# Performance work log

Hardware: AMD Instinct MI355X
Metric: run time of the kernel (lower is better)

Reference implementation:

```python
import jax, jax.numpy as jnp
import numpy as np

DIM = 1024
N_HEADS = 16
HEAD_DIM = DIM // N_HEADS
SCALE = HEAD_DIM ** 0.5


def setup_inputs() -> dict:
    key = jax.random.key(0)
    k_x, k_wqkv, k_bqkv, k_wp, k_bp = jax.random.split(key, 5)
    B, S = 4, 2048
    x = jax.random.normal(k_x, (B, S, DIM), dtype=jnp.float32)
    # Linear params stored input-major: y = x @ W + b
    std_qkv = 1.0 / np.sqrt(DIM)
    W_qkv = jax.random.uniform(k_wqkv, (DIM, 3 * DIM), jnp.float32, -std_qkv, std_qkv)
    b_qkv = jax.random.uniform(k_bqkv, (3 * DIM,), jnp.float32, -std_qkv, std_qkv)
    W_proj = jax.random.uniform(k_wp, (DIM, DIM), jnp.float32, -std_qkv, std_qkv)
    b_proj = jax.random.uniform(k_bp, (DIM,), jnp.float32, -std_qkv, std_qkv)
    return {"x": x, "W_qkv": W_qkv, "b_qkv": b_qkv, "W_proj": W_proj, "b_proj": b_proj}


def reference(x, W_qkv, b_qkv, W_proj, b_proj):
    B, S, D = x.shape
    qkv = x @ W_qkv + b_qkv                       # [B,S,3D]
    Q, K, V = jnp.split(qkv, 3, axis=-1)          # each [B,S,D]
    def heads(t):                                 # [B,S,D] -> [B,H,S,hd]
        return t.reshape(B, S, N_HEADS, HEAD_DIM).transpose(0, 2, 1, 3)
    Q, K, V = heads(Q), heads(K), heads(V)
    scores = jnp.einsum('bhqd,bhkd->bhqk', Q, K) / SCALE   # [B,H,S,S]
    attn = jax.nn.softmax(scores, axis=-1)
    out = jnp.einsum('bhqk,bhkd->bhqd', attn, V)           # [B,H,S,hd]
    out = out.transpose(0, 2, 1, 3).reshape(B, S, D)
    return out @ W_proj + b_proj
```

## Files before the change

### kernel.cpp

```cpp
#include <hip/hip_runtime.h>
#include <hip/hip_bf16.h>

typedef __attribute__((ext_vector_type(8))) __bf16 bf16x8;
typedef __attribute__((ext_vector_type(4))) float f32x4;
typedef __attribute__((ext_vector_type(16))) float f32x16;
typedef __attribute__((ext_vector_type(4))) unsigned int u32x4;

#define DIM 1024
#define NHEADS 16
#define HDIM 64
#define BATCH 4
#define SEQ 2048
#define ROWS (BATCH * SEQ)
#define SCL 0.18033688011112042f

__device__ inline unsigned short f2bf(float f) {
    __hip_bfloat16 h = __float2bfloat16(f);
    return *reinterpret_cast<unsigned short*>(&h);
}

__device__ inline unsigned int packbf2(float a, float b) {
    unsigned short ua = __builtin_bit_cast(unsigned short, (__bf16)a);
    unsigned short ub = __builtin_bit_cast(unsigned short, (__bf16)b);
    return (unsigned int)ua | ((unsigned int)ub << 16);
}

typedef const __attribute__((address_space(1))) unsigned int* gas_ptr;
typedef __attribute__((address_space(3))) unsigned int* las_ptr;
__device__ inline void gload16(const void* g, void* l) {
    __builtin_amdgcn_global_load_lds((gas_ptr)g, (las_ptr)l, 16, 0, 0);
}

__global__ __launch_bounds__(256) void prologue(const float* __restrict__ x,
                                                unsigned short* __restrict__ x_bf,
                                                const float* __restrict__ W_qkv,
                                                unsigned short* __restrict__ WqkvT,
                                                const float* __restrict__ W_proj,
                                                unsigned short* __restrict__ WprojT) {
    __shared__ float tile[32][33];
    const int blk = blockIdx.x;
    if (blk < 8192) {
        int i = blk * 256 + threadIdx.x;
        float4 v = ((const float4*)x)[i];
        ushort4 o;
        o.x = f2bf(v.x); o.y = f2bf(v.y); o.z = f2bf(v.z); o.w = f2bf(v.w);
        ((ushort4*)x_bf)[i] = o;
        return;
    }
    const float* in; unsigned short* outp; int C, srows, bx, byy; float scl;
    if (blk < 11264) {
        int t = blk - 8192;
        in = W_qkv; outp = WqkvT; C = 3 * DIM; srows = DIM; scl = SCL;
        bx = t % 96; byy = t / 96;
    } else {
        int t = blk - 11264;
        in = W_proj; outp = WprojT; C = DIM; srows = 0; scl = 1.f;
        bx = t & 31; byy = t >> 5;
    }
    const int R = DIM;
    int c0 = bx * 32, r0 = byy * 32;
    int tx = threadIdx.x & 31, ty = threadIdx.x >> 5;
#pragma unroll
    for (int i = 0; i < 32; i += 8) {
        int r = r0 + ty + i, c = c0 + tx;
        tile[ty + i][tx] = in[(size_t)r * C + c];
    }
    __syncthreads();
#pragma unroll
    for (int i = 0; i < 32; i += 8) {
        int orow = c0 + ty + i, oc = r0 + tx;
        float v = tile[tx][ty + i];
        if (orow < srows) v *= scl;
        outp[(size_t)orow * R + oc] = f2bf(v);
    }
}

__global__ __launch_bounds__(512, 2) void qkv_gemm_pack(const unsigned short* __restrict__ A,
                                                        const unsigned short* __restrict__ Bt,
                                                        const float* __restrict__ bias,
                                                        unsigned short* __restrict__ Cq,
                                                        unsigned short* __restrict__ Kp,
                                                        unsigned short* __restrict__ Vp) {
    __shared__ __align__(16) char SMEM[131072];
    const int tid = threadIdx.x;
    const int lane = tid & 63, wave = tid >> 6;
    const int wr = wave >> 2, wc = wave & 3;
    const int fr = lane & 15, lh = lane >> 4;
    const int gflat = blockIdx.y * gridDim.x + blockIdx.x;
    const int bidx = (gflat & 7) * 48 + (gflat >> 3);
    const int bx = bidx % 12, byy = bidx / 12;
    const int rowA = byy * 256, colB = bx * 256;

    const int sA = wave * 8 + (lane >> 3);
    const int arow0 = sA;
    const int crow0 = (sA & 31) + (sA >> 5) * 64;
    const int glb = ((lane & 7) ^ (lane >> 3)) * 16;
    const int ga0 = ((lh) ^ (fr & 7)) * 16;
    const int ga1 = ((4 + lh) ^ (fr & 7)) * 16;
    const int aoff = (wr * 64 + fr) * 128;
    const int boff = (wc * 32 + fr) * 128;

    f32x4 acc[8][4] = {};

    auto stA = [&](int tb, int h, int tt) {
        char* d = SMEM + tb * 65536 + h * 16384 + wave * 1024;
        const char* g0 = (const char*)A +
            (((size_t)(rowA + arow0 + h * 64)) * 1024 + (size_t)tt * 64) * 2 + glb;
        gload16(g0, d);
        gload16(g0 + (size_t)128 * 2048, d + 8192);
    };
    auto stB = [&](int tb, int h, int tt) {
        char* d = SMEM + tb * 65536 + 32768 + h * 16384 + wave * 1024;
        const char* g0 = (const char*)Bt +
            (((size_t)(colB + crow0 + h * 32)) * 1024 + (size_t)tt * 64) * 2 + glb;
        gload16(g0, d);
        gload16(g0 + (size_t)128 * 2048, d + 8192);
    };

    stA(0, 0, 0); stB(0, 0, 0); stA(0, 1, 0); stB(0, 1, 0);
    stA(1, 0, 1); stB(1, 0, 1);
    asm volatile("s_waitcnt vmcnt(4)" ::: "memory");
    __builtin_amdgcn_s_barrier();

    bf16x8 afq[4][2];
    for (int u = 0; u < 16; ++u) {
        const int cur = u & 1;
        const char* Al = SMEM + cur * 65536;
        const char* Bl = SMEM + cur * 65536 + 32768;
        {
            bf16x8 bfp[2][2];
#pragma unroll
            for (int i = 0; i < 4; i++) {
                afq[i][0] = *(const bf16x8*)(Al + aoff + i * 2048 + ga0);
                afq[i][1] = *(const bf16x8*)(Al + aoff + i * 2048 + ga1);
            }
#pragma unroll
            for (int j = 0; j < 2; j++) {
                bfp[j][0] = *(const bf16x8*)(Bl + boff + j * 2048 + ga0);
                bfp[j][1] = *(const bf16x8*)(Bl + boff + j * 2048 + ga1);
            }
            if (u + 1 < 16) stA(cur ^ 1, 1, u + 1);
            __builtin_amdgcn_s_barrier();
            __builtin_amdgcn_s_setprio(1);
#pragma unroll
            for (int i = 0; i < 4; i++)
#pragma unroll
                for (int j = 0; j < 2; j++) {
                    acc[i][j] = __builtin_amdgcn_mfma_f32_16x16x32_bf16(afq[i][0], bfp[j][0], acc[i][j], 0, 0, 0);
                    acc[i][j] = __builtin_amdgcn_mfma_f32_16x16x32_bf16(afq[i][1], bfp[j][1], acc[i][j], 0, 0, 0);
                }
            __builtin_amdgcn_s_setprio(0);
            __builtin_amdgcn_s_barrier();
        }
        {
            bf16x8 bfp[2][2];
#pragma unroll
            for (int j = 0; j < 2; j++) {
                bfp[j][0] = *(const bf16x8*)(Bl + 16384 + boff + j * 2048 + ga0);
                bfp[j][1] = *(const bf16x8*)(Bl + 16384 + boff + j * 2048 + ga1);
            }
            if (u + 1 < 16) stB(cur ^ 1, 1, u + 1);
            __builtin_amdgcn_s_barrier();
            __builtin_amdgcn_s_setprio(1);
#pragma unroll
            for (int i = 0; i < 4; i++)
#pragma unroll
                for (int j = 0; j < 2; j++) {
                    acc[i][2 + j] = __builtin_amdgcn_mfma_f32_16x16x32_bf16(afq[i][0], bfp[j][0], acc[i][2 + j], 0, 0, 0);
                    acc[i][2 + j] = __builtin_amdgcn_mfma_f32_16x16x32_bf16(afq[i][1], bfp[j][1], acc[i][2 + j], 0, 0, 0);
                }
            __builtin_amdgcn_s_setprio(0);
            __builtin_amdgcn_s_barrier();
        }
        {
            bf16x8 bfp[2][2];
#pragma unroll
            for (int i = 0; i < 4; i++) {
                afq[i][0] = *(const bf16x8*)(Al + 16384 + aoff + i * 2048 + ga0);
                afq[i][1] = *(const bf16x8*)(Al + 16384 + aoff + i * 2048 + ga1);
            }
#pragma unroll
            for (int j = 0; j < 2; j++) {
                bfp[j][0] = *(const bf16x8*)(Bl + boff + j * 2048 + ga0);
                bfp[j][1] = *(const bf16x8*)(Bl + boff + j * 2048 + ga1);
            }
            if (u + 2 < 16) stA(cur, 0, u + 2);
            __builtin_amdgcn_s_barrier();
            __builtin_amdgcn_s_setprio(1);
#pragma unroll
            for (int i = 0; i < 4; i++)
#pragma unroll
                for (int j = 0; j < 2; j++) {
                    acc[4 + i][j] = __builtin_amdgcn_mfma_f32_16x16x32_bf16(afq[i][0], bfp[j][0], acc[4 + i][j], 0, 0, 0);
                    acc[4 + i][j] = __builtin_amdgcn_mfma_f32_16x16x32_bf16(afq[i][1], bfp[j][1], acc[4 + i][j], 0, 0, 0);
                }
            __builtin_amdgcn_s_setprio(0);
            __builtin_amdgcn_s_barrier();
        }
        {
            bf16x8 bfp[2][2];
#pragma unroll
            for (int j = 0; j < 2; j++) {
                bfp[j][0] = *(const bf16x8*)(Bl + 16384 + boff + j * 2048 + ga0);
                bfp[j][1] = *(const bf16x8*)(Bl + 16384 + boff + j * 2048 + ga1);
            }
            if (u + 2 < 16) stB(cur, 0, u + 2);
            __builtin_amdgcn_s_barrier();
            __builtin_amdgcn_s_setprio(1);
#pragma unroll
            for (int i = 0; i < 4; i++)
#pragma unroll
                for (int j = 0; j < 2; j++) {
                    acc[4 + i][2 + j] = __builtin_amdgcn_mfma_f32_16x16x32_bf16(afq[i][0], bfp[j][0], acc[4 + i][2 + j], 0, 0, 0);
                    acc[4 + i][2 + j] = __builtin_amdgcn_mfma_f32_16x16x32_bf16(afq[i][1], bfp[j][1], acc[4 + i][2 + j], 0, 0, 0);
                }
            __builtin_amdgcn_s_setprio(0);
            if (u < 14) asm volatile("s_waitcnt vmcnt(4)" ::: "memory");
            else        asm volatile("s_waitcnt vmcnt(0)" ::: "memory");
            __builtin_amdgcn_s_barrier();
        }
    }

    const int cm = (lane >> 4) * 4, cn = lane & 15;
    const int gn0 = colB + wc * 64;
    if (gn0 < 1024) {
        for (int ni = 0; ni < 4; ni++) {
            int gn = gn0 + ni * 16 + cn;
            float bv = bias[gn] * SCL;
            for (int mi = 0; mi < 8; mi++) {
#pragma unroll
                for (int r = 0; r < 4; r++) {
                    int gm = rowA + wr * 128 + mi * 16 + cm + r;
                    Cq[(size_t)gm * 1024 + gn] = f2bf(acc[mi][ni][r] + bv);
                }
            }
        }
    } else {
        const int mm = lane & 31, hh = lane >> 5;
        unsigned short* Lw = (unsigned short*)SMEM + wave * (64 * 72);
        for (int kg = 0; kg < 2; kg++) {
            for (int ni = 0; ni < 4; ni++) {
                float bv = bias[gn0 + ni * 16 + cn];
                for (int mi = 0; mi < 4; mi++) {
#pragma unroll
                    for (int r = 0; r < 4; r++)
                        Lw[(mi * 16 + cm + r) * 72 + ni * 16 + cn] =
                            f2bf(acc[kg * 4 + mi][ni][r] + bv);
                }
            }
            __builtin_amdgcn_s_waitcnt(0);
            const int keybase = rowA + wr * 128 + kg * 64;
            const int b = keybase >> 11, s0g = keybase & 2047;
            if (gn0 < 2048) {
                const int h = (gn0 - 1024) >> 6;
                const size_t by = (size_t)(b * 16 + h);
                const int kub = s0g >> 5;
#pragma unroll
                for (int f = 0; f < 8; f++) {
                    int ktl = f >> 2, ks = f & 3;
                    uint4 d = *(const uint4*)&Lw[(ktl * 32 + mm) * 72 + ks * 16 + hh * 8];
                    *(uint4*)(Kp + ((by * 64 + kub + ktl) * 4 + ks) * 512 + lane * 8) = d;
                }
            } else {
                const int h = (gn0 - 2048) >> 6;
                const size_t by = (size_t)(b * 16 + h);
                const int vub = s0g >> 4;
#pragma unroll
                for (int f = 0; f < 8; f++) {
                    int ksl = f >> 1, dt = f & 1;
                    unsigned short tmp[8];
#pragma unroll
                    for (int j = 0; j < 8; j++)
                        tmp[j] = Lw[(ksl * 16 + (j & 3) + 8 * (j >> 2) + 4 * hh) * 72 + dt * 32 + mm];
                    *(uint4*)(Vp + ((by * 128 + vub + ksl) * 2 + dt) * 512 + lane * 8) =
                        *(uint4*)tmp;
                }
            }
            __builtin_amdgcn_s_waitcnt(0);
        }
    }
}

__global__ __launch_bounds__(256) void gemm_bt_bias(const unsigned short* __restrict__ A,
                                                    const unsigned short* __restrict__ Bt,
                                                    const float* __restrict__ bias,
                                                    float* __restrict__ Cf,
                                                    int M, int N, int K) {
    __shared__ unsigned short SMEM[16384];
    unsigned short* As0 = SMEM;
    unsigned short* Bs0 = SMEM + 8192;
    const int tid = threadIdx.x;
    const int lane = tid & 63, wave = tid >> 6;
    const int wm = (wave >> 1) * 64, wn = (wave & 1) * 64;
    const int nwg = gridDim.x * gridDim.y;
    const int gflat = blockIdx.y * gridDim.x + blockIdx.x;
    const int bidx = (gflat & 7) * (nwg >> 3) + (gflat >> 3);
    const int bx = bidx % gridDim.x, byy = bidx / gridDim.x;
    const int rowA = byy * 128, rowB = bx * 128;
    const int fr = lane & 15, fo = (lane >> 4) * 8;

    f32x4 acc[4][4] = {};

    for (int k0 = 0; k0 < K; k0 += 64) {
#pragma unroll
        for (int kc = 0; kc < 2; kc++) {
#pragma unroll
            for (int c = 0; c < 2; c++) {
                int o = c * 4096 + tid * 16;
                int r = o >> 6, cb = o & 63;
                int ldsb = c * 4096 + wave * 1024;
                gload16((const char*)A + ((size_t)(rowA + r) * K + k0 + kc * 32) * 2 + cb,
                        (char*)As0 + kc * 8192 + ldsb);
                gload16((const char*)Bt + ((size_t)(rowB + r) * K + k0 + kc * 32) * 2 + cb,
                        (char*)Bs0 + kc * 8192 + ldsb);
            }
        }
        __syncthreads();
#pragma unroll
        for (int kc = 0; kc < 2; kc++) {
            bf16x8 af[4], bfr[4];
#pragma unroll
            for (int i = 0; i < 4; i++) {
                af[i]  = *(const bf16x8*)(As0 + kc * 4096 + (wm + i * 16 + fr) * 32 + fo);
                bfr[i] = *(const bf16x8*)(Bs0 + kc * 4096 + (wn + i * 16 + fr) * 32 + fo);
            }
#pragma unroll
            for (int mi = 0; mi < 4; mi++)
#pragma unroll
                for (int ni = 0; ni < 4; ni++)
                    acc[mi][ni] = __builtin_amdgcn_mfma_f32_16x16x32_bf16(af[mi], bfr[ni],
                                                                          acc[mi][ni], 0, 0, 0);
        }
        __syncthreads();
    }

    const int cn = lane & 15, cm = (lane >> 4) * 4;
    for (int ni = 0; ni < 4; ni++) {
        int gn = rowB + wn + ni * 16 + cn;
        float bv = bias[gn];
        for (int mi = 0; mi < 4; mi++) {
#pragma unroll
            for (int r = 0; r < 4; r++) {
                int gm = rowA + wm + mi * 16 + cm + r;
                Cf[(size_t)gm * N + gn] = acc[mi][ni][r] + bv;
            }
        }
    }
}

__device__ inline void softmax_pv(const f32x16& cfrag, const bf16x8 vf[2][2],
                                  f32x16& o0, f32x16& o1, float& psum) {
    unsigned int pk[8];
    float es[8];
#pragma unroll
    for (int p = 0; p < 8; p++) {
        float e0 = __builtin_amdgcn_exp2f(cfrag[2 * p]);
        float e1 = __builtin_amdgcn_exp2f(cfrag[2 * p + 1]);
        es[p] = e0 + e1;
        pk[p] = packbf2(e0, e1);
    }
    psum += ((es[0] + es[1]) + (es[2] + es[3])) + ((es[4] + es[5]) + (es[6] + es[7]));
    u32x4 lo = {pk[0], pk[1], pk[2], pk[3]};
    u32x4 hi = {pk[4], pk[5], pk[6], pk[7]};
    bf16x8 pa0 = __builtin_bit_cast(bf16x8, lo);
    bf16x8 pa1 = __builtin_bit_cast(bf16x8, hi);
    o0 = __builtin_amdgcn_mfma_f32_32x32x16_bf16(pa0, vf[0][0], o0, 0, 0, 0);
    o1 = __builtin_amdgcn_mfma_f32_32x32x16_bf16(pa0, vf[0][1], o1, 0, 0, 0);
    o0 = __builtin_amdgcn_mfma_f32_32x32x16_bf16(pa1, vf[1][0], o0, 0, 0, 0);
    o1 = __builtin_amdgcn_mfma_f32_32x32x16_bf16(pa1, vf[1][1], o1, 0, 0, 0);
}

__device__ inline void attn_step(const bf16x8 kf[4], const bf16x8 vf[2][2],
                                 const bf16x8 qf[2][4], f32x16 oacc[2][2], float psum[2]) {
    f32x16 cf0 = {}, cf1 = {};
#pragma unroll
    for (int ks = 0; ks < 4; ks++)
        cf0 = __builtin_amdgcn_mfma_f32_32x32x16_bf16(kf[ks], qf[0][ks], cf0, 0, 0, 0);
#pragma unroll
    for (int ks = 0; ks < 4; ks++)
        cf1 = __builtin_amdgcn_mfma_f32_32x32x16_bf16(kf[ks], qf[1][ks], cf1, 0, 0, 0);
    softmax_pv(cf0, vf, oacc[0][0], oacc[0][1], psum[0]);
    softmax_pv(cf1, vf, oacc[1][0], oacc[1][1], psum[1]);
}

__global__ __launch_bounds__(256, 2) void attn_kernel(const unsigned short* __restrict__ Qb,
                                                      const unsigned short* __restrict__ Kp,
                                                      const unsigned short* __restrict__ Vp,
                                                      unsigned short* __restrict__ attnb) {
    __shared__ float Po[2][8 * 256];
    __shared__ float Pl[2][128];
    const int tid = threadIdx.x;
    const int lane = tid & 63, wave = tid >> 6;
    const int qpair = wave >> 1, ksplit = wave & 1;
    const int m31 = lane & 31, h = lane >> 5;
    const int gflat = blockIdx.y * gridDim.x + blockIdx.x;
    const int xcd = gflat & 7, slot = gflat >> 3;
    const int by = xcd * 8 + (slot >> 4);
    const int qb = slot & 15;
    const int b = by >> 4;
    const int bS = b * SEQ, hcol = (by & 15) * HDIM;
    const int q0 = qb * 128 + qpair * 64;

    bf16x8 qf[2][4];
#pragma unroll
    for (int qt = 0; qt < 2; qt++)
#pragma unroll
        for (int ks = 0; ks < 4; ks++)
            qf[qt][ks] = *(const bf16x8*)(Qb + (size_t)(bS + q0 + qt * 32 + m31) * 1024 +
                                          hcol + ks * 16 + h * 8);

    f32x16 oacc[2][2] = {};
    float psum[2] = {0.f, 0.f};

    const unsigned short* kbase = Kp + (size_t)by * 64 * 2048 + lane * 8;
    const unsigned short* vbase = Vp + (size_t)by * 128 * 1024 + lane * 8;

    const int ku0 = ksplit * 32;
    bf16x8 kfa[4], kfb[4];
    {
        const unsigned short* kp = kbase + (size_t)ku0 * 2048;
#pragma unroll
        for (int ks = 0; ks < 4; ks++) kfa[ks] = *(const bf16x8*)(kp + ks * 512);
    }
    for (int ki = 0; ki < 32; ki += 2) {
        {
            int ku = ku0 + ki;
            bf16x8 vf[2][2];
#pragma unroll
            for (int ks = 0; ks < 2; ks++) {
                const unsigned short* vp = vbase + ((size_t)ku * 2 + ks) * 1024;
                vf[ks][0] = *(const bf16x8*)(vp);
                vf[ks][1] = *(const bf16x8*)(vp + 512);
            }
            const unsigned short* kpn = kbase + (size_t)(ku + 1) * 2048;
#pragma unroll
            for (int ks = 0; ks < 4; ks++) kfb[ks] = *(const bf16x8*)(kpn + ks * 512);
            attn_step(kfa, vf, qf, oacc, psum);
        }
        {
            int ku = ku0 + ki + 1;
            bf16x8 vf[2][2];
#pragma unroll
            for (int ks = 0; ks < 2; ks++) {
                const unsigned short* vp = vbase + ((size_t)ku * 2 + ks) * 1024;
                vf[ks][0] = *(const bf16x8*)(vp);
                vf[ks][1] = *(const bf16x8*)(vp + 512);
            }
            int kup = ku0 + ((ki + 2 < 32) ? (ki + 2) : 31);
            const unsigned short* kpn = kbase + (size_t)kup * 2048;
#pragma unroll
            for (int ks = 0; ks < 4; ks++) kfa[ks] = *(const bf16x8*)(kpn + ks * 512);
            attn_step(kfb, vf, qf, oacc, psum);
        }
    }

#pragma unroll
    for (int qt = 0; qt < 2; qt++) {
        if (ksplit == 1) {
#pragma unroll
            for (int dt = 0; dt < 2; dt++)
#pragma unroll
                for (int c = 0; c < 4; c++) {
                    f32x4 v = {oacc[qt][dt][c * 4 + 0], oacc[qt][dt][c * 4 + 1],
                               oacc[qt][dt][c * 4 + 2], oacc[qt][dt][c * 4 + 3]};
                    *(f32x4*)&Po[qpair][(dt * 4 + c) * 256 + lane * 4] = v;
                }
            if (qt == 0)
                *(float2*)&Pl[qpair][lane * 2] = make_float2(psum[0], psum[1]);
        }
        __syncthreads();
        if (ksplit == 0) {
#pragma unroll
            for (int dt = 0; dt < 2; dt++)
#pragma unroll
                for (int c = 0; c < 4; c++) {
                    f32x4 v = *(const f32x4*)&Po[qpair][(dt * 4 + c) * 256 + lane * 4];
#pragma unroll
                    for (int j = 0; j < 4; j++) oacc[qt][dt][c * 4 + j] += v[j];
                }
            if (qt == 0) {
                float2 pl = *(const float2*)&Pl[qpair][lane * 2];
                psum[0] += pl.x; psum[1] += pl.y;
            }
        }
        if (qt == 0) __syncthreads();
    }

    if (ksplit == 0) {
#pragma unroll
        for (int qt = 0; qt < 2; qt++) {
            float lt = psum[qt] + __shfl_xor(psum[qt], 32, 64);
            float rl = 1.f / lt;
#pragma unroll
            for (int r = 0; r < 16; r++) {
                int row = (r & 3) + 8 * (r >> 2) + 4 * h;
                float rlr = __shfl(rl, row, 64);
                size_t orow = (size_t)(bS + q0 + qt * 32 + row) * 1024 + hcol;
                attnb[orow + m31]      = f2bf(oacc[qt][0][r] * rlr);
                attnb[orow + 32 + m31] = f2bf(oacc[qt][1][r] * rlr);
            }
        }
    }
}

extern "C" void kernel_launch(void* const* d_in, const int* in_sizes, int n_in,
                              void* d_out, int out_size, void* d_ws, size_t ws_size,
                              hipStream_t stream) {
    const float* x      = (const float*)d_in[0];
    const float* W_qkv  = (const float*)d_in[1];
    const float* b_qkv  = (const float*)d_in[2];
    const float* W_proj = (const float*)d_in[3];
    const float* b_proj = (const float*)d_in[4];
    float* out = (float*)d_out;

    char* ws = (char*)d_ws;
    unsigned short* x_bf   = (unsigned short*)(ws);
    unsigned short* WqkvT  = (unsigned short*)(ws + 16777216);
    unsigned short* Qb     = (unsigned short*)(ws + 23068672);
    unsigned short* Kp     = (unsigned short*)(ws + 39845888);
    unsigned short* Vp     = (unsigned short*)(ws + 56623104);
    unsigned short* WprojT = (unsigned short*)(ws + 73400320);
    unsigned short* attnb  = (unsigned short*)(ws);

    prologue<<<12288, 256, 0, stream>>>(x, x_bf, W_qkv, WqkvT, W_proj, WprojT);

    qkv_gemm_pack<<<dim3(12, 32), 512, 0, stream>>>(x_bf, WqkvT, b_qkv, Qb, Kp, Vp);

    attn_kernel<<<dim3(SEQ / 128, BATCH * NHEADS), 256, 0, stream>>>(Qb, Kp, Vp, attnb);

    gemm_bt_bias<<<dim3(DIM / 128, ROWS / 128), 256, 0, stream>>>(
        attnb, WprojT, b_proj, out, ROWS, DIM, DIM);
}
```

Measured before the change: 257.3 us.

## Unify QKV and output-projection GEMMs into one pipelined 256x128-tile kernel

The QKV GEMM tile shrinks from 256x256 to 256x128, with 8 waves laid out 4x2 and 96KB of LDS, which doubles the QKV grid to 24x32 workgroups. The same software-pipelined kernel now also runs the output projection (8x32 grid, fp32 output plus bias), replacing the simpler non-pipelined 128x128 gemm_bt_bias. The goals are better CU occupancy and load balance for the QKV GEMM, and a faster output projection through double-buffered async loads. The trade-off is lower per-tile data reuse.

```diff
diff --git a/kernel.cpp b/kernel.cpp
--- a/kernel.cpp
+++ b/kernel.cpp
@@ -75,62 +75,62 @@
     }
 }
 
-__global__ __launch_bounds__(512, 2) void qkv_gemm_pack(const unsigned short* __restrict__ A,
-                                                        const unsigned short* __restrict__ Bt,
-                                                        const float* __restrict__ bias,
-                                                        unsigned short* __restrict__ Cq,
-                                                        unsigned short* __restrict__ Kp,
-                                                        unsigned short* __restrict__ Vp) {
-    __shared__ __align__(16) char SMEM[131072];
+__global__ __launch_bounds__(512, 2) void gemm_pipe(const unsigned short* __restrict__ A,
+                                                    const unsigned short* __restrict__ Bt,
+                                                    const float* __restrict__ bias,
+                                                    unsigned short* __restrict__ Cq,
+                                                    unsigned short* __restrict__ Kp,
+                                                    unsigned short* __restrict__ Vp,
+                                                    float* __restrict__ Cf, int N) {
+    __shared__ __align__(16) char SMEM[98304];
     const int tid = threadIdx.x;
     const int lane = tid & 63, wave = tid >> 6;
-    const int wr = wave >> 2, wc = wave & 3;
+    const int wr = wave >> 1, wc = wave & 1;
     const int fr = lane & 15, lh = lane >> 4;
+    const int nwg = gridDim.x * gridDim.y;
     const int gflat = blockIdx.y * gridDim.x + blockIdx.x;
-    const int bidx = (gflat & 7) * 48 + (gflat >> 3);
-    const int bx = bidx % 12, byy = bidx / 12;
-    const int rowA = byy * 256, colB = bx * 256;
+    const int bidx = (gflat & 7) * (nwg >> 3) + (gflat >> 3);
+    const int bx = bidx % gridDim.x, byy = bidx / gridDim.x;
+    const int rowA = byy * 256, colB = bx * 128;
 
     const int sA = wave * 8 + (lane >> 3);
-    const int arow0 = sA;
-    const int crow0 = (sA & 31) + (sA >> 5) * 64;
+    const int pr0 = (sA & 31) + (sA >> 5) * 64;
     const int glb = ((lane & 7) ^ (lane >> 3)) * 16;
     const int ga0 = ((lh) ^ (fr & 7)) * 16;
     const int ga1 = ((4 + lh) ^ (fr & 7)) * 16;
-    const int aoff = (wr * 64 + fr) * 128;
+    const int aoff = (wr * 32 + fr) * 128;
     const int boff = (wc * 32 + fr) * 128;
 
-    f32x4 acc[8][4] = {};
+    f32x4 acc[4][4] = {};
 
     auto stA = [&](int tb, int h, int tt) {
-        char* d = SMEM + tb * 65536 + h * 16384 + wave * 1024;
+        char* d = SMEM + tb * 49152 + h * 16384 + wave * 1024;
         const char* g0 = (const char*)A +
-            (((size_t)(rowA + arow0 + h * 64)) * 1024 + (size_t)tt * 64) * 2 + glb;
+            (((size_t)(rowA + pr0 + h * 32)) * 1024 + (size_t)tt * 64) * 2 + glb;
         gload16(g0, d);
         gload16(g0 + (size_t)128 * 2048, d + 8192);
     };
     auto stB = [&](int tb, int h, int tt) {
-        char* d = SMEM + tb * 65536 + 32768 + h * 16384 + wave * 1024;
+        char* d = SMEM + tb * 49152 + 32768 + h * 8192 + wave * 1024;
         const char* g0 = (const char*)Bt +
-            (((size_t)(colB + crow0 + h * 32)) * 1024 + (size_t)tt * 64) * 2 + glb;
+            (((size_t)(colB + pr0 + h * 32)) * 1024 + (size_t)tt * 64) * 2 + glb;
         gload16(g0, d);
-        gload16(g0 + (size_t)128 * 2048, d + 8192);
     };
 
-    stA(0, 0, 0); stB(0, 0, 0); stA(0, 1, 0); stB(0, 1, 0);
+    stA(0, 0, 0); stA(0, 1, 0); stB(0, 0, 0); stB(0, 1, 0);
     stA(1, 0, 1); stB(1, 0, 1);
-    asm volatile("s_waitcnt vmcnt(4)" ::: "memory");
+    asm volatile("s_waitcnt vmcnt(3)" ::: "memory");
     __builtin_amdgcn_s_barrier();
 
-    bf16x8 afq[4][2];
+    bf16x8 afq[2][2];
     for (int u = 0; u < 16; ++u) {
         const int cur = u & 1;
-        const char* Al = SMEM + cur * 65536;
-        const char* Bl = SMEM + cur * 65536 + 32768;
+        const char* Al = SMEM + cur * 49152;
+        const char* Bl = SMEM + cur * 49152 + 32768;
         {
             bf16x8 bfp[2][2];
 #pragma unroll
-            for (int i = 0; i < 4; i++) {
+            for (int i = 0; i < 2; i++) {
                 afq[i][0] = *(const bf16x8*)(Al + aoff + i * 2048 + ga0);
                 afq[i][1] = *(const bf16x8*)(Al + aoff + i * 2048 + ga1);
             }
@@ -143,7 +143,7 @@
             __builtin_amdgcn_s_barrier();
             __builtin_amdgcn_s_setprio(1);
 #pragma unroll
-            for (int i = 0; i < 4; i++)
+            for (int i = 0; i < 2; i++)
 #pragma unroll
                 for (int j = 0; j < 2; j++) {
                     acc[i][j] = __builtin_amdgcn_mfma_f32_16x16x32_bf16(afq[i][0], bfp[j][0], acc[i][j], 0, 0, 0);
@@ -156,14 +156,14 @@
             bf16x8 bfp[2][2];
 #pragma unroll
             for (int j = 0; j < 2; j++) {
-                bfp[j][0] = *(const bf16x8*)(Bl + 16384 + boff + j * 2048 + ga0);
-                bfp[j][1] = *(const bf16x8*)(Bl + 16384 + boff + j * 2048 + ga1);
+                bfp[j][0] = *(const bf16x8*)(Bl + 8192 + boff + j * 2048 + ga0);
+                bfp[j][1] = *(const bf16x8*)(Bl + 8192 + boff + j * 2048 + ga1);
             }
             if (u + 1 < 16) stB(cur ^ 1, 1, u + 1);
             __builtin_amdgcn_s_barrier();
             __builtin_amdgcn_s_setprio(1);
 #pragma unroll
-            for (int i = 0; i < 4; i++)
+            for (int i = 0; i < 2; i++)
 #pragma unroll
                 for (int j = 0; j < 2; j++) {
                     acc[i][2 + j] = __builtin_amdgcn_mfma_f32_16x16x32_bf16(afq[i][0], bfp[j][0], acc[i][2 + j], 0, 0, 0);
@@ -175,7 +175,7 @@
         {
             bf16x8 bfp[2][2];
 #pragma unroll
-            for (int i = 0; i < 4; i++) {
+            for (int i = 0; i < 2; i++) {
                 afq[i][0] = *(const bf16x8*)(Al + 16384 + aoff + i * 2048 + ga0);
                 afq[i][1] = *(const bf16x8*)(Al + 16384 + aoff + i * 2048 + ga1);
             }
@@ -188,11 +188,11 @@
             __builtin_amdgcn_s_barrier();
             __builtin_amdgcn_s_setprio(1);
 #pragma unroll
-            for (int i = 0; i < 4; i++)
+            for (int i = 0; i < 2; i++)
 #pragma unroll
                 for (int j = 0; j < 2; j++) {
-                    acc[4 + i][j] = __builtin_amdgcn_mfma_f32_16x16x32_bf16(afq[i][0], bfp[j][0], acc[4 + i][j], 0, 0, 0);
-                    acc[4 + i][j] = __builtin_amdgcn_mfma_f32_16x16x32_bf16(afq[i][1], bfp[j][1], acc[4 + i][j], 0, 0, 0);
+                    acc[2 + i][j] = __builtin_amdgcn_mfma_f32_16x16x32_bf16(afq[i][0], bfp[j][0], acc[2 + i][j], 0, 0, 0);
+                    acc[2 + i][j] = __builtin_amdgcn_mfma_f32_16x16x32_bf16(afq[i][1], bfp[j][1], acc[2 + i][j], 0, 0, 0);
                 }
             __builtin_amdgcn_s_setprio(0);
             __builtin_amdgcn_s_barrier();
@@ -201,21 +201,21 @@
             bf16x8 bfp[2][2];
 #pragma unroll
             for (int j = 0; j < 2; j++) {
-                bfp[j][0] = *(const bf16x8*)(Bl + 16384 + boff + j * 2048 + ga0);
-                bfp[j][1] = *(const bf16x8*)(Bl + 16384 + boff + j * 2048 + ga1);
+                bfp[j][0] = *(const bf16x8*)(Bl + 8192 + boff + j * 2048 + ga0);
+                bfp[j][1] = *(const bf16x8*)(Bl + 8192 + boff + j * 2048 + ga1);
             }
             if (u + 2 < 16) stB(cur, 0, u + 2);
             __builtin_amdgcn_s_barrier();
             __builtin_amdgcn_s_setprio(1);
 #pragma unroll
-            for (int i = 0; i < 4; i++)
+            for (int i = 0; i < 2; i++)
 #pragma unroll
                 for (int j = 0; j < 2; j++) {
-                    acc[4 + i][2 + j] = __builtin_amdgcn_mfma_f32_16x16x32_bf16(afq[i][0], bfp[j][0], acc[4 + i][2 + j], 0, 0, 0);
-                    acc[4 + i][2 + j] = __builtin_amdgcn_mfma_f32_16x16x32_bf16(afq[i][1], bfp[j][1], acc[4 + i][2 + j], 0, 0, 0);
+                    acc[2 + i][2 + j] = __builtin_amdgcn_mfma_f32_16x16x32_bf16(afq[i][0], bfp[j][0], acc[2 + i][2 + j], 0, 0, 0);
+                    acc[2 + i][2 + j] = __builtin_amdgcn_mfma_f32_16x16x32_bf16(afq[i][1], bfp[j][1], acc[2 + i][2 + j], 0, 0, 0);
                 }
             __builtin_amdgcn_s_setprio(0);
-            if (u < 14) asm volatile("s_waitcnt vmcnt(4)" ::: "memory");
+            if (u < 14) asm volatile("s_waitcnt vmcnt(3)" ::: "memory");
             else        asm volatile("s_waitcnt vmcnt(0)" ::: "memory");
             __builtin_amdgcn_s_barrier();
         }
@@ -223,126 +223,63 @@
 
     const int cm = (lane >> 4) * 4, cn = lane & 15;
     const int gn0 = colB + wc * 64;
-    if (gn0 < 1024) {
+    const int gm0 = rowA + wr * 64;
+    if (Cf) {
+        for (int ni = 0; ni < 4; ni++) {
+            int gn = gn0 + ni * 16 + cn;
+            float bv = bias[gn];
+            for (int mi = 0; mi < 4; mi++) {
+#pragma unroll
+                for (int r = 0; r < 4; r++)
+                    Cf[(size_t)(gm0 + mi * 16 + cm + r) * N + gn] = acc[mi][ni][r] + bv;
+            }
+        }
+    } else if (gn0 < 1024) {
         for (int ni = 0; ni < 4; ni++) {
             int gn = gn0 + ni * 16 + cn;
             float bv = bias[gn] * SCL;
-            for (int mi = 0; mi < 8; mi++) {
-#pragma unroll
-                for (int r = 0; r < 4; r++) {
-                    int gm = rowA + wr * 128 + mi * 16 + cm + r;
-                    Cq[(size_t)gm * 1024 + gn] = f2bf(acc[mi][ni][r] + bv);
-                }
+            for (int mi = 0; mi < 4; mi++) {
+#pragma unroll
+                for (int r = 0; r < 4; r++)
+                    Cq[(size_t)(gm0 + mi * 16 + cm + r) * 1024 + gn] = f2bf(acc[mi][ni][r] + bv);
             }
         }
     } else {
         const int mm = lane & 31, hh = lane >> 5;
         unsigned short* Lw = (unsigned short*)SMEM + wave * (64 * 72);
-        for (int kg = 0; kg < 2; kg++) {
-            for (int ni = 0; ni < 4; ni++) {
-                float bv = bias[gn0 + ni * 16 + cn];
-                for (int mi = 0; mi < 4; mi++) {
-#pragma unroll
-                    for (int r = 0; r < 4; r++)
-                        Lw[(mi * 16 + cm + r) * 72 + ni * 16 + cn] =
-                            f2bf(acc[kg * 4 + mi][ni][r] + bv);
-                }
-            }
-            __builtin_amdgcn_s_waitcnt(0);
-            const int keybase = rowA + wr * 128 + kg * 64;
-            const int b = keybase >> 11, s0g = keybase & 2047;
-            if (gn0 < 2048) {
-                const int h = (gn0 - 1024) >> 6;
-                const size_t by = (size_t)(b * 16 + h);
-                const int kub = s0g >> 5;
-#pragma unroll
-                for (int f = 0; f < 8; f++) {
-                    int ktl = f >> 2, ks = f & 3;
-                    uint4 d = *(const uint4*)&Lw[(ktl * 32 + mm) * 72 + ks * 16 + hh * 8];
-                    *(uint4*)(Kp + ((by * 64 + kub + ktl) * 4 + ks) * 512 + lane * 8) = d;
-                }
-            } else {
-                const int h = (gn0 - 2048) >> 6;
-                const size_t by = (size_t)(b * 16 + h);
-                const int vub = s0g >> 4;
-#pragma unroll
-                for (int f = 0; f < 8; f++) {
-                    int ksl = f >> 1, dt = f & 1;
-                    unsigned short tmp[8];
-#pragma unroll
-                    for (int j = 0; j < 8; j++)
-                        tmp[j] = Lw[(ksl * 16 + (j & 3) + 8 * (j >> 2) + 4 * hh) * 72 + dt * 32 + mm];
-                    *(uint4*)(Vp + ((by * 128 + vub + ksl) * 2 + dt) * 512 + lane * 8) =
-                        *(uint4*)tmp;
-                }
-            }
-            __builtin_amdgcn_s_waitcnt(0);
-        }
-    }
-}
-
-__global__ __launch_bounds__(256) void gemm_bt_bias(const unsigned short* __restrict__ A,
-                                                    const unsigned short* __restrict__ Bt,
-                                                    const float* __restrict__ bias,
-                                                    float* __restrict__ Cf,
-                                                    int M, int N, int K) {
-    __shared__ unsigned short SMEM[16384];
-    unsigned short* As0 = SMEM;
-    unsigned short* Bs0 = SMEM + 8192;
-    const int tid = threadIdx.x;
-    const int lane = tid & 63, wave = tid >> 6;
-    const int wm = (wave >> 1) * 64, wn = (wave & 1) * 64;
-    const int nwg = gridDim.x * gridDim.y;
-    const int gflat = blockIdx.y * gridDim.x + blockIdx.x;
-    const int bidx = (gflat & 7) * (nwg >> 3) + (gflat >> 3);
-    const int bx = bidx % gridDim.x, byy = bidx / gridDim.x;
-    const int rowA = byy * 128, rowB = bx * 128;
-    const int fr = lane & 15, fo = (lane >> 4) * 8;
-
-    f32x4 acc[4][4] = {};
-
-    for (int k0 = 0; k0 < K; k0 += 64) {
-#pragma unroll
-        for (int kc = 0; kc < 2; kc++) {
-#pragma unroll
-            for (int c = 0; c < 2; c++) {
-                int o = c * 4096 + tid * 16;
-                int r = o >> 6, cb = o & 63;
-                int ldsb = c * 4096 + wave * 1024;
-                gload16((const char*)A + ((size_t)(rowA + r) * K + k0 + kc * 32) * 2 + cb,
-                        (char*)As0 + kc * 8192 + ldsb);
-                gload16((const char*)Bt + ((size_t)(rowB + r) * K + k0 + kc * 32) * 2 + cb,
-                        (char*)Bs0 + kc * 8192 + ldsb);
-            }
-        }
-        __syncthreads();
-#pragma unroll
-        for (int kc = 0; kc < 2; kc++) {
-            bf16x8 af[4], bfr[4];
-#pragma unroll
-            for (int i = 0; i < 4; i++) {
-                af[i]  = *(const bf16x8*)(As0 + kc * 4096 + (wm + i * 16 + fr) * 32 + fo);
-                bfr[i] = *(const bf16x8*)(Bs0 + kc * 4096 + (wn + i * 16 + fr) * 32 + fo);
-            }
-#pragma unroll
-            for (int mi = 0; mi < 4; mi++)
-#pragma unroll
-                for (int ni = 0; ni < 4; ni++)
-                    acc[mi][ni] = __builtin_amdgcn_mfma_f32_16x16x32_bf16(af[mi], bfr[ni],
-                                                                          acc[mi][ni], 0, 0, 0);
-        }
-        __syncthreads();
-    }
-
-    const int cn = lane & 15, cm = (lane >> 4) * 4;
-    for (int ni = 0; ni < 4; ni++) {
-        int gn = rowB + wn + ni * 16 + cn;
-        float bv = bias[gn];
-        for (int mi = 0; mi < 4; mi++) {
-#pragma unroll
-            for (int r = 0; r < 4; r++) {
-                int gm = rowA + wm + mi * 16 + cm + r;
-                Cf[(size_t)gm * N + gn] = acc[mi][ni][r] + bv;
+        for (int ni = 0; ni < 4; ni++) {
+            float bv = bias[gn0 + ni * 16 + cn];
+            for (int mi = 0; mi < 4; mi++) {
+#pragma unroll
+                for (int r = 0; r < 4; r++)
+                    Lw[(mi * 16 + cm + r) * 72 + ni * 16 + cn] = f2bf(acc[mi][ni][r] + bv);
+            }
+        }
+        __builtin_amdgcn_s_waitcnt(0);
+        const int b = gm0 >> 11, s0g = gm0 & 2047;
+        if (gn0 < 2048) {
+            const int h = (gn0 - 1024) >> 6;
+            const size_t by = (size_t)(b * 16 + h);
+            const int kub = s0g >> 5;
+#pragma unroll
+            for (int f = 0; f < 8; f++) {
+                int ktl = f >> 2, ks = f & 3;
+                uint4 d = *(const uint4*)&Lw[(ktl * 32 + mm) * 72 + ks * 16 + hh * 8];
+                *(uint4*)(Kp + ((by * 64 + kub + ktl) * 4 + ks) * 512 + lane * 8) = d;
+            }
+        } else {
+            const int h = (gn0 - 2048) >> 6;
+            const size_t by = (size_t)(b * 16 + h);
+            const int vub = s0g >> 4;
+#pragma unroll
+            for (int f = 0; f < 8; f++) {
+                int ksl = f >> 1, dt = f & 1;
+                unsigned short tmp[8];
+#pragma unroll
+                for (int j = 0; j < 8; j++)
+                    tmp[j] = Lw[(ksl * 16 + (j & 3) + 8 * (j >> 2) + 4 * hh) * 72 + dt * 32 + mm];
+                *(uint4*)(Vp + ((by * 128 + vub + ksl) * 2 + dt) * 512 + lane * 8) =
+                    *(uint4*)tmp;
             }
         }
     }
@@ -524,10 +461,11 @@
 
     prologue<<<12288, 256, 0, stream>>>(x, x_bf, W_qkv, WqkvT, W_proj, WprojT);
 
-    qkv_gemm_pack<<<dim3(12, 32), 512, 0, stream>>>(x_bf, WqkvT, b_qkv, Qb, Kp, Vp);
+    gemm_pipe<<<dim3(24, 32), 512, 0, stream>>>(x_bf, WqkvT, b_qkv, Qb, Kp, Vp,
+                                                nullptr, 3 * DIM);
 
     attn_kernel<<<dim3(SEQ / 128, BATCH * NHEADS), 256, 0, stream>>>(Qb, Kp, Vp, attnb);
 
-    gemm_bt_bias<<<dim3(DIM / 128, ROWS / 128), 256, 0, stream>>>(
-        attnb, WprojT, b_proj, out, ROWS, DIM, DIM);
-}
+    gemm_pipe<<<dim3(8, 32), 512, 0, stream>>>(attnb, WprojT, b_proj, nullptr, nullptr,
+                                               nullptr, out, DIM);
+}
```

Result: no change. 258.9 us (+0.6%).
